# Optimization experiments

Measured on AMD Instinct MI355X. Metric: run time of the kernel, lower is better.

## Reference

```python
import jax, jax.numpy as jnp
import numpy as np

L, H = 3, 8
B, N, D, E = 4, 256, 128, 128
NH, EH1, EH2 = 512, 512, 512


def _ln(x, g, b):
    m = x.mean(-1, keepdims=True)
    v = ((x - m) ** 2).mean(-1, keepdims=True)
    return (x - m) * jax.lax.rsqrt(v + 1e-5) * g + b


def setup_inputs() -> dict:
    key = jax.random.key(0)
    ks = jax.random.split(key, 16)
    w = lambda k, *s: jax.random.normal(k, s, jnp.float32) * 0.02
    inp = {
        'node_features': jax.random.normal(ks[0], (B, N, D), jnp.float32),
        'edge_features': jax.random.normal(ks[1], (B, N, N, E), jnp.float32),
        'Wqkv_n': w(ks[2], L, D, 3 * D), 'bqkv_n': jnp.zeros((L, 3 * D)),
        'Wqkv_e': w(ks[3], L, E, 3 * D), 'bqkv_e': jnp.zeros((L, 3 * D)),
        'Wo': w(ks[4], L, D, D), 'bo': jnp.zeros((L, D)),
        'Wn1': w(ks[5], L, D, NH), 'bn1': jnp.zeros((L, NH)),
        'Wn2': w(ks[6], L, NH, D), 'bn2': jnp.zeros((L, D)),
        'ln1n_g': jnp.ones((L, D)), 'ln1n_b': jnp.zeros((L, D)),
        'ln2n_g': jnp.ones((L, D)), 'ln2n_b': jnp.zeros((L, D)),
        'We1a': w(ks[7], L, 2 * D + 2 * E, EH1), 'be1a': jnp.zeros((L, EH1)),
        'We1b': w(ks[8], L, EH1, E), 'be1b': jnp.zeros((L, E)),
        'We2a': w(ks[9], L, E, EH2), 'be2a': jnp.zeros((L, EH2)),
        'We2b': w(ks[10], L, EH2, E), 'be2b': jnp.zeros((L, E)),
        'ln1e_g': jnp.ones((L, E)), 'ln1e_b': jnp.zeros((L, E)),
        'ln2e_g': jnp.ones((L, E)), 'ln2e_b': jnp.zeros((L, E)),
    }
    return inp


def reference(node_features, edge_features, Wqkv_n, bqkv_n, Wqkv_e, bqkv_e, Wo, bo,
              Wn1, bn1, Wn2, bn2, ln1n_g, ln1n_b, ln2n_g, ln2n_b,
              We1a, be1a, We1b, be1b, We2a, be2a, We2b, be2b,
              ln1e_g, ln1e_b, ln2e_g, ln2e_b):
    n, e = node_features, edge_features
    b_, N_, D_ = n.shape
    hd = D_ // H
    scale = 1.0 / np.sqrt(hd).astype(np.float32)
    for l in range(Wqkv_n.shape[0]):
        # ---- edge-biased attention ----
        qkv_n = (n @ Wqkv_n[l] + bqkv_n[l]).reshape(b_, N_, H, 3 * hd).transpose(0, 2, 1, 3)  # B,H,N,3hd
        q_n, k_n, v_n = jnp.split(qkv_n, 3, axis=-1)
        qkv_e = (e @ Wqkv_e[l] + bqkv_e[l]).reshape(b_, N_, N_, H, 3 * hd).transpose(0, 3, 1, 2, 4)  # B,H,N,N,3hd
        q_e, k_e, v_e = jnp.split(qkv_e, 3, axis=-1)
        q = q_n[:, :, :, None, :] + q_e  # B,H,N,N,hd
        # NOTE: the original torch code overwrites k with q (`k = q.reshape(...)`),
        # so scores are the squared norm of q; k_n/k_e are dead code. Faithful.
        scores = jnp.einsum('bhijd,bhijd->bhij', q, q) * scale
        att = jax.nn.softmax(scores, axis=-1)
        v = v_n[:, :, None, :, :] + v_e  # B,H,N,N,hd
        out = jnp.einsum('bhij,bhijd->bhid', att, v)  # B,H,N,hd
        out = out.transpose(0, 2, 1, 3).reshape(b_, N_, D_) @ Wo[l] + bo[l]
        n = _ln(n + out, ln1n_g[l], ln1n_b[l])
        ff = jax.nn.relu(n @ Wn1[l] + bn1[l]) @ Wn2[l] + bn2[l]
        n = _ln(n + ff, ln2n_g[l], ln2n_b[l])
        # ---- edge update ----
        src = jnp.broadcast_to(n[:, None, :, :], (b_, N_, N_, D_))  # node j
        tgt = jnp.broadcast_to(n[:, :, None, :], (b_, N_, N_, D_))  # node i
        cat = jnp.concatenate([e, e.transpose(0, 2, 1, 3), src, tgt], axis=-1)
        e1 = jax.nn.relu(cat @ We1a[l] + be1a[l]) @ We1b[l] + be1b[l]
        e = _ln(e + e1, ln1e_g[l], ln1e_b[l])
        e2 = jax.nn.relu(e @ We2a[l] + be2a[l]) @ We2b[l] + be2b[l]
        e = _ln(e + e2, ln2e_g[l], ln2e_b[l])
    return n
```

## Files before the change

kernel.cpp:

```cpp
#include <hip/hip_runtime.h>

typedef unsigned short u16;
typedef __bf16 bf16x8 __attribute__((ext_vector_type(8)));
typedef float f32x4 __attribute__((ext_vector_type(4)));

#define NB 4
#define NN 256
#define DD 128
#define RNN 262144

__device__ __forceinline__ u16 f2b(float f) {
    unsigned u = __builtin_bit_cast(unsigned, f);
    unsigned rb = ((u >> 16) & 1u) + 0x7FFFu;
    return (u16)((u + rb) >> 16);
}
__device__ __forceinline__ float b2f(u16 u) {
    return __builtin_bit_cast(float, ((unsigned)u) << 16);
}

__device__ __forceinline__ void glds16(const void* g, void* l) {
    __builtin_amdgcn_global_load_lds((const __attribute__((address_space(1))) void*)g,
                                     (__attribute__((address_space(3))) void*)l, 16, 0, 0);
}

__global__ void prep_weights(const float* __restrict__ Wqkv_e, const float* __restrict__ bqkv_e,
                             const float* __restrict__ We1a, const float* __restrict__ We1b,
                             const float* __restrict__ We2a, const float* __restrict__ We2b,
                             u16* wqT, u16* wv, float* bqp, float* bvp,
                             u16* we1aT, u16* we1bT, u16* we2aT, u16* we2bT) {
    int l = blockIdx.z, sec = blockIdx.y;
    int idx = blockIdx.x * 256 + threadIdx.x;
    if (sec == 0) {
        if (idx < 16384) {
            int n = idx >> 7, k = idx & 127;
            int col = (n >> 4) * 48 + (n & 15);
            wqT[l * 16384 + n * 128 + k] = f2b(Wqkv_e[l * 49152 + k * 384 + col]);
        }
    } else if (sec == 1) {
        if (idx < 16384) {
            int k = idx >> 7, c = idx & 127;
            int col = (c >> 4) * 48 + 32 + (c & 15);
            wv[l * 16384 + k * 128 + c] = f2b(Wqkv_e[l * 49152 + k * 384 + col]);
        }
        if (idx < 128) {
            bqp[l * 128 + idx] = bqkv_e[l * 384 + (idx >> 4) * 48 + (idx & 15)];
            bvp[l * 128 + idx] = bqkv_e[l * 384 + (idx >> 4) * 48 + 32 + (idx & 15)];
        }
    } else if (sec == 2) {
        if (idx < 131072) {
            int n = idx >> 8, k = idx & 255;
            we1aT[l * 131072 + n * 256 + k] = f2b(We1a[l * 262144 + k * 512 + n]);
        }
    } else if (sec == 3) {
        if (idx < 65536) {
            int n = idx >> 9, k = idx & 511;
            we1bT[l * 65536 + n * 512 + k] = f2b(We1b[l * 65536 + k * 128 + n]);
        }
    } else if (sec == 4) {
        if (idx < 65536) {
            int n = idx >> 7, k = idx & 127;
            we2aT[l * 65536 + n * 128 + k] = f2b(We2a[l * 65536 + k * 512 + n]);
        }
    } else {
        if (idx < 65536) {
            int n = idx >> 9, k = idx & 511;
            we2bT[l * 65536 + n * 512 + k] = f2b(We2b[l * 65536 + k * 128 + n]);
        }
    }
}

__global__ void init_e(const float4* __restrict__ src, ushort4* __restrict__ dst) {
    const long n4 = 8388608;
    for (long i = (long)blockIdx.x * blockDim.x + threadIdx.x; i < n4; i += (long)gridDim.x * blockDim.x) {
        float4 v = src[i];
        ushort4 o;
        o.x = f2b(v.x); o.y = f2b(v.y); o.z = f2b(v.z); o.w = f2b(v.w);
        dst[i] = o;
    }
}

__global__ void init_n(const float* __restrict__ node, float* __restrict__ nf) {
    int i = blockIdx.x * 256 + threadIdx.x;
    if (i < 131072) nf[i] = node[i];
}

__launch_bounds__(512)
__global__ void pre_node_kernel(const float* __restrict__ nf, const float* __restrict__ We1a,
                                float* __restrict__ preS, float* __restrict__ preT) {
    __shared__ float nr[128];
    int tid = threadIdx.x;
    int row = blockIdx.x;
    if (tid < 128) nr[tid] = nf[(long)row * 128 + tid];
// ... 159 lines not shown
        g_s[(h0 + 6) * 128 + k] = a3;
    }
    __syncthreads();
    {
        int c = tid & 127, half = tid >> 7;
        int h = c >> 4;
        float a = 0.f;
        for (int j = half * 128; j < half * 128 + 128; ++j)
            a += s_s[h * 256 + j] * vn[((long)(b * NN + j)) * 128 + c];
        for (int k = half * 64; k < half * 64 + 64; ++k)
            a += g_s[h * 128 + k] * b2f(Wv[k * 128 + c]);
        part[tid] = a;
    }
    __syncthreads();
    if (tid < 128)
        attn_o[((long)(b * NN + i)) * 128 + tid] = part[tid] + part[128 + tid] + bvp[tid];
}

__launch_bounds__(256)
__global__ void node_kernel(const float* __restrict__ attn_o, float* __restrict__ nf,
                            const float* __restrict__ Wo, const float* __restrict__ bo,
                            const float* __restrict__ Wn1, const float* __restrict__ bn1,
                            const float* __restrict__ Wn2, const float* __restrict__ bn2,
                            const float* __restrict__ g1, const float* __restrict__ b1,
                            const float* __restrict__ g2, const float* __restrict__ b2) {
    __shared__ float ao[128], nr[128], n1[128], hb[512];
    __shared__ float red[8];
    int tid = threadIdx.x;
    int wid = tid >> 6, lane = tid & 63;
    long base = (long)blockIdx.x * 128;
    if (tid < 128) { ao[tid] = attn_o[base + tid]; nr[tid] = nf[base + tid]; }
    __syncthreads();
    float x = 0.f;
    if (tid < 128) {
        float a = bo[tid];
        #pragma unroll 8
        for (int k = 0; k < 128; ++k) a += ao[k] * Wo[k * 128 + tid];
        x = nr[tid] + a;
    }
    float s = (tid < 128) ? x : 0.f, q = (tid < 128) ? x * x : 0.f;
    #pragma unroll
    for (int mk = 1; mk <= 32; mk <<= 1) { s += __shfl_xor(s, mk); q += __shfl_xor(q, mk); }
    if (lane == 0) { red[wid * 2] = s; red[wid * 2 + 1] = q; }
    __syncthreads();
    float sum = red[0] + red[2] + red[4] + red[6];
    float sq  = red[1] + red[3] + red[5] + red[7];
    float mean = sum * (1.f / 128.f);
    float var = sq * (1.f / 128.f) - mean * mean;
    float rs = rsqrtf(var + 1e-5f);
    __syncthreads();
    if (tid < 128) n1[tid] = (x - mean) * rs * g1[tid] + b1[tid];
    __syncthreads();
    for (int c = tid; c < 512; c += 256) {
        float a = bn1[c];
        #pragma unroll 8
        for (int k = 0; k < 128; ++k) a += n1[k] * Wn1[k * 512 + c];
        hb[c] = a > 0.f ? a : 0.f;
    }
    __syncthreads();
    float y = 0.f;
    if (tid < 128) {
        float a = bn2[tid];
        #pragma unroll 8
        for (int k = 0; k < 512; ++k) a += hb[k] * Wn2[k * 128 + tid];
        y = n1[tid] + a;
    }
    float s2 = (tid < 128) ? y : 0.f, q2 = (tid < 128) ? y * y : 0.f;
    #pragma unroll
    for (int mk = 1; mk <= 32; mk <<= 1) { s2 += __shfl_xor(s2, mk); q2 += __shfl_xor(q2, mk); }
    if (lane == 0) { red[wid * 2] = s2; red[wid * 2 + 1] = q2; }
    __syncthreads();
    sum = red[0] + red[2] + red[4] + red[6];
    sq  = red[1] + red[3] + red[5] + red[7];
    mean = sum * (1.f / 128.f);
    var = sq * (1.f / 128.f) - mean * mean;
    rs = rsqrtf(var + 1e-5f);
    if (tid < 128) {
        float o = (y - mean) * rs * g2[tid] + b2[tid];
        nf[base + tid] = o;
    }
}

template<int KT1, int CAT>
__launch_bounds__(256, 2)
__global__ void fused_mlp2(const u16* __restrict__ W1T, const float* __restrict__ b1v,
                           const u16* __restrict__ W2T, const float* __restrict__ b2v,
                           const u16* __restrict__ ein, const u16* __restrict__ Aplain,
                           const u16* __restrict__ e_res,
                           const float* __restrict__ preS, const float* __restrict__ preT,
                           const float* __restrict__ lng, const float* __restrict__ lnb,
                           u16* __restrict__ e_dst) {
    __shared__ u16 A_lds[KT1 * 4096];
    __shared__ u16 Ws[8192];
    __shared__ u16 Hs[8192];

    const int K1 = KT1 * 64;
    int tid = threadIdx.x;
    int wid = tid >> 6, lane = tid & 63;
    long row0 = (long)blockIdx.x * 64;
    int b = (int)(row0 >> 16);
    int rem0 = (int)(row0 & 65535);
    int i_ = rem0 >> 8, j0 = rem0 & 255;
    int wn = wid >> 1, wrr = wid & 1;
    int wr2 = wid >> 1, wc2 = wid & 1;

    #pragma unroll
    for (int kt = 0; kt < KT1; ++kt) {
        #pragma unroll
        for (int p = 0; p < 2; ++p) {
            int r = p * 32 + (tid >> 3);
            int ch = tid & 7;
            const u16* src;
            if (CAT) {
                int seg = kt >> 1;
                int off = ((kt & 1) << 6) + ((ch ^ (r & 7)) << 3);
                long ridx = seg == 0 ? (long)(b * NN + i_) * NN + (j0 + r)
                                     : (long)(b * NN + (j0 + r)) * NN + i_;
                src = ein + ridx * DD + off;
            } else {
                src = Aplain + (row0 + r) * K1 + (kt << 6) + ((ch ^ (r & 7)) << 3);
            }
            glds16(src, (char*)A_lds + kt * 8192 + (p << 12) + (wid << 10));
        }
    }

    f32x4 z = {0.f, 0.f, 0.f, 0.f};
    f32x4 acc2[2][4];
    #pragma unroll
    for (int m = 0; m < 2; ++m)
        #pragma unroll
        for (int n = 0; n < 4; ++n) acc2[m][n] = z;

    for (int q = 0; q < 4; ++q) {
        int nq0 = q << 7;
        f32x4 acc1[4][2];
        #pragma unroll
        for (int mn = 0; mn < 4; ++mn) { acc1[mn][0] = z; acc1[mn][1] = z; }

        #pragma unroll
        for (int kt = 0; kt < KT1; ++kt) {
            #pragma unroll
            for (int pp = 0; pp < 4; ++pp) {
                int n = pp * 32 + (tid >> 3);
                int ch = tid & 7;
                const u16* src = W1T + (long)(nq0 + n) * K1 + (kt << 6) + ((ch ^ (n & 7)) << 3);
                glds16(src, (char*)Ws + (pp << 12) + (wid << 10));
            }
            __syncthreads();
            #pragma unroll
            for (int ks = 0; ks < 2; ++ks) {
                bf16x8 af[4], bfr[2];
                #pragma unroll
                for (int mn = 0; mn < 4; ++mn) {
                    int n = wn * 64 + mn * 16 + (lane & 15);
                    int ch = (ks * 4 + (lane >> 4)) ^ (n & 7);
                    af[mn] = *reinterpret_cast<const bf16x8*>(&Ws[n * 64 + ch * 8]);
                }
                #pragma unroll
                for (int mr = 0; mr < 2; ++mr) {
                    int r = wrr * 32 + mr * 16 + (lane & 15);
                    int ch = (ks * 4 + (lane >> 4)) ^ (r & 7);
                    bfr[mr] = *reinterpret_cast<const bf16x8*>(&A_lds[kt * 4096 + r * 64 + ch * 8]);
                }
                #pragma unroll
                for (int mn = 0; mn < 4; ++mn)
                    #pragma unroll
                    for (int mr = 0; mr < 2; ++mr)
                        acc1[mn][mr] = __builtin_amdgcn_mfma_f32_16x16x32_bf16(af[mn], bfr[mr], acc1[mn][mr], 0, 0, 0);
            }
            __syncthreads();
        }

        if (q == 3) {
            #pragma unroll
            for (int p = 0; p < 4; ++p) {
                int rr = p * 16 + (tid >> 4);
                const u16* src = e_res + (row0 + rr) * DD + ((tid & 15) << 3);
                glds16(src, (char*)A_lds + (p << 12) + (wid << 10));
            }
        }

        #pragma unroll
        for (int mn = 0; mn < 4; ++mn) {
            #pragma unroll
            for (int mr = 0; mr < 2; ++mr) {
                int nl0 = wn * 64 + mn * 16 + ((lane >> 4) << 2);
                int n0g = nq0 + nl0;
                int r = wrr * 32 + mr * 16 + (lane & 15);
                float4 bb = *reinterpret_cast<const float4*>(&b1v[n0g]);
                if (CAT) {
                    float4 pt = *reinterpret_cast<const float4*>(&preT[(long)(b * NN + i_) * 512 + n0g]);
                    float4 ps = *reinterpret_cast<const float4*>(&preS[(long)(b * NN + j0 + r) * 512 + n0g]);
                    bb.x += pt.x + ps.x; bb.y += pt.y + ps.y;
                    bb.z += pt.z + ps.z; bb.w += pt.w + ps.w;
                }
                float v0 = acc1[mn][mr][0] + bb.x; v0 = v0 > 0.f ? v0 : 0.f;
                float v1 = acc1[mn][mr][1] + bb.y; v1 = v1 > 0.f ? v1 : 0.f;
                float v2 = acc1[mn][mr][2] + bb.z; v2 = v2 > 0.f ? v2 : 0.f;
                float v3 = acc1[mn][mr][3] + bb.w; v3 = v3 > 0.f ? v3 : 0.f;
                uint2 pk;
                pk.x = (unsigned)f2b(v0) | ((unsigned)f2b(v1) << 16);
                pk.y = (unsigned)f2b(v2) | ((unsigned)f2b(v3) << 16);
                int c8 = nl0 >> 3;
                int cs = (c8 & 8) | ((c8 ^ r) & 7);
                *reinterpret_cast<uint2*>((char*)Hs + r * 256 + cs * 16 + (nl0 & 7) * 2) = pk;
            }
        }

        #pragma unroll
        for (int kt2 = 0; kt2 < 2; ++kt2) {
            #pragma unroll
            for (int pp = 0; pp < 4; ++pp) {
                int c = pp * 32 + (tid >> 3);
                int ch = tid & 7;
                const u16* src = W2T + (long)c * 512 + nq0 + (kt2 << 6) + ((ch ^ (c & 7)) << 3);
                glds16(src, (char*)Ws + (pp << 12) + (wid << 10));
            }
            __syncthreads();
            #pragma unroll
            for (int ks = 0; ks < 2; ++ks) {
                bf16x8 af2[2], bf2[4];
                #pragma unroll
                for (int m = 0; m < 2; ++m) {
                    int r = wr2 * 32 + m * 16 + (lane & 15);
                    int lk = kt2 * 64 + ks * 32 + ((lane >> 4) << 3);
                    int c8 = lk >> 3;
                    int cs = (c8 & 8) | ((c8 ^ r) & 7);
                    af2[m] = *reinterpret_cast<const bf16x8*>((char*)Hs + r * 256 + cs * 16);
                }
                #pragma unroll
                for (int n = 0; n < 4; ++n) {
                    int c = wc2 * 64 + n * 16 + (lane & 15);
                    int ch = (ks * 4 + (lane >> 4)) ^ (c & 7);
                    bf2[n] = *reinterpret_cast<const bf16x8*>(&Ws[c * 64 + ch * 8]);
                }
                #pragma unroll
                for (int m = 0; m < 2; ++m)
                    #pragma unroll
                    for (int n = 0; n < 4; ++n)
                        acc2[m][n] = __builtin_amdgcn_mfma_f32_16x16x32_bf16(af2[m], bf2[n], acc2[m][n], 0, 0, 0);
            }
            __syncthreads();
        }
    }

    float* psum = (float*)Hs;
    float* psq  = psum + 128;
    u16* eres_lds = A_lds;
    #pragma unroll
    for (int m = 0; m < 2; ++m) {
        float sv[4], qv[4];
        #pragma unroll
        for (int t = 0; t < 4; ++t) { sv[t] = 0.f; qv[t] = 0.f; }
        #pragma unroll
        for (int n = 0; n < 4; ++n) {
            int col = wc2 * 64 + n * 16 + (lane & 15);
            float bb = b2v[col];
            #pragma unroll
            for (int t = 0; t < 4; ++t) {
                int row = wr2 * 32 + m * 16 + ((lane >> 4) << 2) + t;
                float xv = acc2[m][n][t] + bb + b2f(eres_lds[row * 128 + col]);
                acc2[m][n][t] = xv;
                sv[t] += xv;
                qv[t] += xv * xv;
            }
        }
        #pragma unroll
        for (int mk = 1; mk <= 8; mk <<= 1)
            #pragma unroll
            for (int t = 0; t < 4; ++t) { sv[t] += __shfl_xor(sv[t], mk); qv[t] += __shfl_xor(qv[t], mk); }
        if ((lane & 15) == 0) {
            #pragma unroll
            for (int t = 0; t < 4; ++t) {
                int row = wr2 * 32 + m * 16 + ((lane >> 4) << 2) + t;
                psum[row * 2 + wc2] = sv[t];
                psq[row * 2 + wc2] = qv[t];
            }
        }
    }
    __syncthreads();
    #pragma unroll
    for (int m = 0; m < 2; ++m) {
        #pragma unroll
        for (int t = 0; t < 4; ++t) {
            int row = wr2 * 32 + m * 16 + ((lane >> 4) << 2) + t;
            float sum = psum[row * 2] + psum[row * 2 + 1];
            float sq  = psq[row * 2] + psq[row * 2 + 1];
            float mean = sum * (1.f / 128.f);
            float var = sq * (1.f / 128.f) - mean * mean;
            float rs = rsqrtf(var + 1e-5f);
            #pragma unroll
            for (int n = 0; n < 4; ++n) {
                int col = wc2 * 64 + n * 16 + (lane & 15);
                float o = (acc2[m][n][t] - mean) * rs * lng[col] + lnb[col];
                eres_lds[row * 128 + col] = f2b(o);
            }
        }
    }
    __syncthreads();
    #pragma unroll
    for (int p = 0; p < 4; ++p) {
        ulonglong2 v = *reinterpret_cast<const ulonglong2*>((char*)A_lds + (p << 12) + tid * 16);
        *reinterpret_cast<ulonglong2*>((char*)e_dst + row0 * 256 + (p << 12) + tid * 16) = v;
    }
}

extern "C" void kernel_launch(void* const* d_in, const int* in_sizes, int n_in,
                              void* d_out, int out_size, void* d_ws, size_t ws_size,
                              hipStream_t stream) {
    (void)in_sizes; (void)n_in; (void)out_size; (void)ws_size;
    const float* node   = (const float*)d_in[0];
    const float* edge   = (const float*)d_in[1];
    const float* Wqkv_n = (const float*)d_in[2];
    const float* bqkv_n = (const float*)d_in[3];
    const float* Wqkv_e = (const float*)d_in[4];
    const float* bqkv_e = (const float*)d_in[5];
    const float* Wo     = (const float*)d_in[6];
    const float* bo     = (const float*)d_in[7];
    const float* Wn1    = (const float*)d_in[8];
    const float* bn1    = (const float*)d_in[9];
    const float* Wn2    = (const float*)d_in[10];
    const float* bn2    = (const float*)d_in[11];
    const float* ln1n_g = (const float*)d_in[12];
    const float* ln1n_b = (const float*)d_in[13];
    const float* ln2n_g = (const float*)d_in[14];
    const float* ln2n_b = (const float*)d_in[15];
    const float* We1a   = (const float*)d_in[16];
    const float* be1a   = (const float*)d_in[17];
    const float* We1b   = (const float*)d_in[18];
    const float* be1b   = (const float*)d_in[19];
    const float* We2a   = (const float*)d_in[20];
    const float* be2a   = (const float*)d_in[21];
    const float* We2b   = (const float*)d_in[22];
    const float* be2b   = (const float*)d_in[23];
    const float* ln1e_g = (const float*)d_in[24];
    const float* ln1e_b = (const float*)d_in[25];
    const float* ln2e_g = (const float*)d_in[26];
    const float* ln2e_b = (const float*)d_in[27];

    size_t off = 0;
    char* wsb = (char*)d_ws;
    auto alloc = [&](size_t bytes) -> void* {
        void* p = wsb + off;
        off = (off + bytes + 255) & ~(size_t)255;
        return p;
    };
    u16* eb0      = (u16*)alloc((size_t)RNN * 128 * 2);
    u16* eb1      = (u16*)alloc((size_t)RNN * 128 * 2);
    float* scoresp= (float*)alloc((size_t)2097152 * 4);
    float* qn     = (float*)alloc(131072 * 4);
    float* vn     = (float*)alloc(131072 * 4);
    float* attn_o = (float*)alloc(131072 * 4);
    float* nf     = (float*)alloc(131072 * 4);
    float* preS   = (float*)alloc((size_t)1024 * 512 * 4);
    float* preT   = (float*)alloc((size_t)1024 * 512 * 4);
    u16* wqT      = (u16*)alloc(3 * 16384 * 2);
    u16* wv       = (u16*)alloc(3 * 16384 * 2);
    float* bqp    = (float*)alloc(3 * 128 * 4);
    float* bvp    = (float*)alloc(3 * 128 * 4);
    u16* we1aT    = (u16*)alloc(3 * 131072ull * 2);
    u16* we1bT    = (u16*)alloc(3 * 65536 * 2);
    u16* we2aT    = (u16*)alloc(3 * 65536 * 2);
    u16* we2bT    = (u16*)alloc(3 * 65536 * 2);

    {
        dim3 g(1024, 6, 3);
        prep_weights<<<g, 256, 0, stream>>>(Wqkv_e, bqkv_e, We1a, We1b, We2a, We2b,
                                            wqT, wv, bqp, bvp, we1aT, we1bT, we2aT, we2bT);
    }
    init_e<<<2048, 256, 0, stream>>>((const float4*)edge, (ushort4*)eb0);
    init_n<<<512, 256, 0, stream>>>(node, nf);

    for (int l = 0; l < 3; ++l) {
        u16* ein  = (l & 1) ? eb1 : eb0;
        u16* eout = (l & 1) ? eb0 : eb1;
        qkvn_kernel<<<1024, 256, 0, stream>>>(nf, Wqkv_n + l * 49152, bqkv_n + l * 384, qn, vn);
        scores_kernel<<<2048, 256, 0, stream>>>(ein, wqT + l * 16384, bqp + l * 128, qn, scoresp);
        attn_pv_kernel<<<1024, 256, 0, stream>>>(scoresp, ein, vn, wv + l * 16384, bvp + l * 128, attn_o);
        node_kernel<<<1024, 256, 0, stream>>>(attn_o, nf,
                                              Wo + l * 16384, bo + l * 128,
                                              Wn1 + l * 65536, bn1 + l * 512,
                                              Wn2 + l * 65536, bn2 + l * 128,
                                              ln1n_g + l * 128, ln1n_b + l * 128,
                                              ln2n_g + l * 128, ln2n_b + l * 128);
        pre_node_kernel<<<1024, 512, 0, stream>>>(nf, We1a + (size_t)l * 262144, preS, preT);
        fused_mlp2<4, 1><<<4096, 256, 0, stream>>>(we1aT + l * 131072, be1a + l * 512,
                                                   we1bT + l * 65536, be1b + l * 128,
                                                   ein, nullptr, ein, preS, preT,
                                                   ln1e_g + l * 128, ln1e_b + l * 128, eout);
        fused_mlp2<2, 0><<<4096, 256, 0, stream>>>(we2aT + l * 65536, be2a + l * 512,
                                                   we2bT + l * 65536, be2b + l * 128,
                                                   nullptr, eout, eout, nullptr, nullptr,
                                                   ln2e_g + l * 128, ln2e_b + l * 128, eout);
    }
    hipMemcpyAsync(d_out, nf, 131072 * sizeof(float), hipMemcpyDeviceToDevice, stream);
}
```

Measured before the change: 1.531 ms.

## Pipeline edge MLP weight tiles through triple-buffered LDS with interleaved GEMM phases

Rewrites the fused two-layer edge MLP kernel to stream weight tiles in 64-wide halves through a 3-stage LDS ring buffer. The next tile's global-to-LDS load is issued before computing on the current one, which hides load latency and cuts the barriers that used to bracket every tile. The residual is now read from the already-loaded input tile instead of being reloaded. Smaller LDS (half-size hidden buffer) allows 3 blocks/CU for the second MLP. The cost is more complex staging logic and more, finer-grained syncs.

```diff
diff --git a/kernel.cpp b/kernel.cpp
--- a/kernel.cpp
+++ b/kernel.cpp
@@ -8,6 +8,8 @@
 #define NN 256
 #define DD 128
 #define RNN 262144
+
+template<int N> struct IC { static constexpr int v = N; };
 
 __device__ __forceinline__ u16 f2b(float f) {
     unsigned u = __builtin_bit_cast(unsigned, f);
@@ -333,189 +335,217 @@
 }
 
 template<int KT1, int CAT>
-__launch_bounds__(256, 2)
-__global__ void fused_mlp2(const u16* __restrict__ W1T, const float* __restrict__ b1v,
+__launch_bounds__(256, (KT1 == 4) ? 2 : 3)
+__global__ void fused_mlp3(const u16* __restrict__ W1T, const float* __restrict__ b1v,
                            const u16* __restrict__ W2T, const float* __restrict__ b2v,
                            const u16* __restrict__ ein, const u16* __restrict__ Aplain,
-                           const u16* __restrict__ e_res,
                            const float* __restrict__ preS, const float* __restrict__ preT,
                            const float* __restrict__ lng, const float* __restrict__ lnb,
                            u16* __restrict__ e_dst) {
-    __shared__ u16 A_lds[KT1 * 4096];
-    __shared__ u16 Ws[8192];
-    __shared__ u16 Hs[8192];
-
-    const int K1 = KT1 * 64;
+    __shared__ __align__(16) u16 A_lds[KT1 * 4096];
+    __shared__ __align__(16) u16 ws[3 * 4096];
+    __shared__ __align__(16) u16 Hs[4096];
+
+    constexpr int K1 = KT1 * 64;
     int tid = threadIdx.x;
     int wid = tid >> 6, lane = tid & 63;
     long row0 = (long)blockIdx.x * 64;
     int b = (int)(row0 >> 16);
     int rem0 = (int)(row0 & 65535);
     int i_ = rem0 >> 8, j0 = rem0 & 255;
-    int wn = wid >> 1, wrr = wid & 1;
-    int wr2 = wid >> 1, wc2 = wid & 1;
-
-    #pragma unroll
-    for (int kt = 0; kt < KT1; ++kt) {
-        #pragma unroll
-        for (int p = 0; p < 2; ++p) {
-            int r = p * 32 + (tid >> 3);
+    int wa = wid >> 1, wb = wid & 1;
+
+    int stg = 0, rdS = 0;
+
+    auto SW1 = [&](int qq, int kt, int nh) {
+        char* dst = (char*)ws + stg * 8192; stg = (stg + 1) % 3;
+        #pragma unroll
+        for (int pp = 0; pp < 2; ++pp) {
+            int nl = pp * 32 + (tid >> 3);
+            int ch = tid & 7;
+            const u16* src = W1T + (long)((qq << 7) + nh * 64 + nl) * K1 + (kt << 6) + ((ch ^ (nl & 7)) << 3);
+            glds16(src, dst + (pp << 12) + (wid << 10));
+        }
+    };
+    auto SW2 = [&](int qq, int nh, int ch2) {
+        char* dst = (char*)ws + stg * 8192; stg = (stg + 1) % 3;
+        #pragma unroll
+        for (int pp = 0; pp < 2; ++pp) {
+            int cl = pp * 32 + (tid >> 3);
+            int ch = tid & 7;
+            const u16* src = W2T + (long)(ch2 * 64 + cl) * 512 + (qq << 7) + nh * 64 + ((ch ^ (cl & 7)) << 3);
+            glds16(src, dst + (pp << 12) + (wid << 10));
+        }
+    };
+
+    f32x4 z = {0.f, 0.f, 0.f, 0.f};
+    f32x4 acc1[2][2][2], acc2[2][2][2];
+    #pragma unroll
+    for (int a = 0; a < 2; ++a)
+        #pragma unroll
+        for (int m = 0; m < 2; ++m)
+            #pragma unroll
+            for (int n = 0; n < 2; ++n) { acc1[a][m][n] = z; acc2[a][m][n] = z; }
+
+    #pragma unroll
+    for (int kt = 0; kt < KT1; ++kt)
+        #pragma unroll
+        for (int pp = 0; pp < 2; ++pp) {
+            int r = pp * 32 + (tid >> 3);
             int ch = tid & 7;
             const u16* src;
-            if (CAT) {
-                int seg = kt >> 1;
-                int off = ((kt & 1) << 6) + ((ch ^ (r & 7)) << 3);
-                long ridx = seg == 0 ? (long)(b * NN + i_) * NN + (j0 + r)
+            if constexpr (CAT) {
+                long ridx = (kt < 2) ? (long)(b * NN + i_) * NN + (j0 + r)
                                      : (long)(b * NN + (j0 + r)) * NN + i_;
-                src = ein + ridx * DD + off;
+                src = ein + ridx * DD + ((kt & 1) << 6) + ((ch ^ (r & 7)) << 3);
             } else {
                 src = Aplain + (row0 + r) * K1 + (kt << 6) + ((ch ^ (r & 7)) << 3);
             }
-            glds16(src, (char*)A_lds + kt * 8192 + (p << 12) + (wid << 10));
-        }
-    }
-
-    f32x4 z = {0.f, 0.f, 0.f, 0.f};
-    f32x4 acc2[2][4];
-    #pragma unroll
-    for (int m = 0; m < 2; ++m)
-        #pragma unroll
-        for (int n = 0; n < 4; ++n) acc2[m][n] = z;
-
-    for (int q = 0; q < 4; ++q) {
+            glds16(src, (char*)A_lds + kt * 8192 + (pp << 12) + (wid << 10));
+        }
+    SW1(0, 0, 0);
+    SW1(0, 0, 1);
+    __syncthreads();
+
+    auto G1c = [&](int kt, auto nhc) {
+        constexpr int nh = decltype(nhc)::v;
+        const u16* w = ws + rdS * 4096; rdS = (rdS + 1) % 3;
+        #pragma unroll
+        for (int ks = 0; ks < 2; ++ks) {
+            bf16x8 af[2], bfr[2];
+            #pragma unroll
+            for (int mn = 0; mn < 2; ++mn) {
+                int nl = wa * 32 + mn * 16 + (lane & 15);
+                int ch = (ks * 4 + (lane >> 4)) ^ (nl & 7);
+                af[mn] = *reinterpret_cast<const bf16x8*>(&w[nl * 64 + ch * 8]);
+            }
+            #pragma unroll
+            for (int mr = 0; mr < 2; ++mr) {
+                int r = wb * 32 + mr * 16 + (lane & 15);
+                int ch = (ks * 4 + (lane >> 4)) ^ (r & 7);
+                bfr[mr] = *reinterpret_cast<const bf16x8*>(&A_lds[kt * 4096 + r * 64 + ch * 8]);
+            }
+            #pragma unroll
+            for (int mn = 0; mn < 2; ++mn)
+                #pragma unroll
+                for (int mr = 0; mr < 2; ++mr)
+                    acc1[nh][mn][mr] = __builtin_amdgcn_mfma_f32_16x16x32_bf16(af[mn], bfr[mr], acc1[nh][mn][mr], 0, 0, 0);
+        }
+    };
+
+    auto EPIc = [&](auto nhc, int q) {
+        constexpr int nh = decltype(nhc)::v;
         int nq0 = q << 7;
-        f32x4 acc1[4][2];
-        #pragma unroll
-        for (int mn = 0; mn < 4; ++mn) { acc1[mn][0] = z; acc1[mn][1] = z; }
-
-        #pragma unroll
-        for (int kt = 0; kt < KT1; ++kt) {
-            #pragma unroll
-            for (int pp = 0; pp < 4; ++pp) {
-                int n = pp * 32 + (tid >> 3);
-                int ch = tid & 7;
-                const u16* src = W1T + (long)(nq0 + n) * K1 + (kt << 6) + ((ch ^ (n & 7)) << 3);
-                glds16(src, (char*)Ws + (pp << 12) + (wid << 10));
-            }
-            __syncthreads();
-            #pragma unroll
-            for (int ks = 0; ks < 2; ++ks) {
-                bf16x8 af[4], bfr[2];
-                #pragma unroll
-                for (int mn = 0; mn < 4; ++mn) {
-                    int n = wn * 64 + mn * 16 + (lane & 15);
-                    int ch = (ks * 4 + (lane >> 4)) ^ (n & 7);
-                    af[mn] = *reinterpret_cast<const bf16x8*>(&Ws[n * 64 + ch * 8]);
+        #pragma unroll
+        for (int mn = 0; mn < 2; ++mn) {
+            int nl0 = wa * 32 + mn * 16 + ((lane >> 4) << 2);
+            int n0g = nq0 + nh * 64 + nl0;
+            float4 bb = *reinterpret_cast<const float4*>(&b1v[n0g]);
+            if constexpr (CAT) {
+                float4 pt = *reinterpret_cast<const float4*>(&preT[(long)(b * NN + i_) * 512 + n0g]);
+                bb.x += pt.x; bb.y += pt.y; bb.z += pt.z; bb.w += pt.w;
+            }
+            #pragma unroll
+            for (int mr = 0; mr < 2; ++mr) {
+                int r = wb * 32 + mr * 16 + (lane & 15);
+                float b0 = bb.x, b1_ = bb.y, b2_ = bb.z, b3 = bb.w;
+                if constexpr (CAT) {
+                    float4 ps = *reinterpret_cast<const float4*>(&preS[(long)(b * NN + j0 + r) * 512 + n0g]);
+                    b0 += ps.x; b1_ += ps.y; b2_ += ps.z; b3 += ps.w;
                 }
-                #pragma unroll
-                for (int mr = 0; mr < 2; ++mr) {
-                    int r = wrr * 32 + mr * 16 + (lane & 15);
-                    int ch = (ks * 4 + (lane >> 4)) ^ (r & 7);
-                    bfr[mr] = *reinterpret_cast<const bf16x8*>(&A_lds[kt * 4096 + r * 64 + ch * 8]);
-                }
-                #pragma unroll
-                for (int mn = 0; mn < 4; ++mn)
-                    #pragma unroll
-                    for (int mr = 0; mr < 2; ++mr)
-                        acc1[mn][mr] = __builtin_amdgcn_mfma_f32_16x16x32_bf16(af[mn], bfr[mr], acc1[mn][mr], 0, 0, 0);
-            }
-            __syncthreads();
-        }
-
-        if (q == 3) {
-            #pragma unroll
-            for (int p = 0; p < 4; ++p) {
-                int rr = p * 16 + (tid >> 4);
-                const u16* src = e_res + (row0 + rr) * DD + ((tid & 15) << 3);
-                glds16(src, (char*)A_lds + (p << 12) + (wid << 10));
-            }
-        }
-
-        #pragma unroll
-        for (int mn = 0; mn < 4; ++mn) {
-            #pragma unroll
-            for (int mr = 0; mr < 2; ++mr) {
-                int nl0 = wn * 64 + mn * 16 + ((lane >> 4) << 2);
-                int n0g = nq0 + nl0;
-                int r = wrr * 32 + mr * 16 + (lane & 15);
-                float4 bb = *reinterpret_cast<const float4*>(&b1v[n0g]);
-                if (CAT) {
-                    float4 pt = *reinterpret_cast<const float4*>(&preT[(long)(b * NN + i_) * 512 + n0g]);
-                    float4 ps = *reinterpret_cast<const float4*>(&preS[(long)(b * NN + j0 + r) * 512 + n0g]);
-                    bb.x += pt.x + ps.x; bb.y += pt.y + ps.y;
-                    bb.z += pt.z + ps.z; bb.w += pt.w + ps.w;
-                }
-                float v0 = acc1[mn][mr][0] + bb.x; v0 = v0 > 0.f ? v0 : 0.f;
-                float v1 = acc1[mn][mr][1] + bb.y; v1 = v1 > 0.f ? v1 : 0.f;
-                float v2 = acc1[mn][mr][2] + bb.z; v2 = v2 > 0.f ? v2 : 0.f;
-                float v3 = acc1[mn][mr][3] + bb.w; v3 = v3 > 0.f ? v3 : 0.f;
+                float v0 = acc1[nh][mn][mr][0] + b0; v0 = v0 > 0.f ? v0 : 0.f;
+                float v1 = acc1[nh][mn][mr][1] + b1_; v1 = v1 > 0.f ? v1 : 0.f;
+                float v2 = acc1[nh][mn][mr][2] + b2_; v2 = v2 > 0.f ? v2 : 0.f;
+                float v3 = acc1[nh][mn][mr][3] + b3; v3 = v3 > 0.f ? v3 : 0.f;
                 uint2 pk;
                 pk.x = (unsigned)f2b(v0) | ((unsigned)f2b(v1) << 16);
                 pk.y = (unsigned)f2b(v2) | ((unsigned)f2b(v3) << 16);
                 int c8 = nl0 >> 3;
-                int cs = (c8 & 8) | ((c8 ^ r) & 7);
-                *reinterpret_cast<uint2*>((char*)Hs + r * 256 + cs * 16 + (nl0 & 7) * 2) = pk;
-            }
-        }
-
-        #pragma unroll
-        for (int kt2 = 0; kt2 < 2; ++kt2) {
-            #pragma unroll
-            for (int pp = 0; pp < 4; ++pp) {
-                int c = pp * 32 + (tid >> 3);
-                int ch = tid & 7;
-                const u16* src = W2T + (long)c * 512 + nq0 + (kt2 << 6) + ((ch ^ (c & 7)) << 3);
-                glds16(src, (char*)Ws + (pp << 12) + (wid << 10));
-            }
-            __syncthreads();
-            #pragma unroll
-            for (int ks = 0; ks < 2; ++ks) {
-                bf16x8 af2[2], bf2[4];
+                int cs = (c8 ^ (r & 7)) & 7;
+                *reinterpret_cast<uint2*>((char*)Hs + r * 128 + cs * 16 + (nl0 & 7) * 2) = pk;
+                acc1[nh][mn][mr] = z;
+            }
+        }
+    };
+
+    auto G2c = [&](auto chc) {
+        constexpr int ch2 = decltype(chc)::v;
+        const u16* w = ws + rdS * 4096; rdS = (rdS + 1) % 3;
+        #pragma unroll
+        for (int ks = 0; ks < 2; ++ks) {
+            bf16x8 af2[2], bf2[2];
+            #pragma unroll
+            for (int mr = 0; mr < 2; ++mr) {
+                int r = wb * 32 + mr * 16 + (lane & 15);
+                int c8 = ks * 4 + (lane >> 4);
+                int cs = (c8 ^ (r & 7)) & 7;
+                af2[mr] = *reinterpret_cast<const bf16x8*>((const char*)Hs + r * 128 + cs * 16);
+            }
+            #pragma unroll
+            for (int mn = 0; mn < 2; ++mn) {
+                int cl = wa * 32 + mn * 16 + (lane & 15);
+                int chn = (ks * 4 + (lane >> 4)) ^ (cl & 7);
+                bf2[mn] = *reinterpret_cast<const bf16x8*>(&w[cl * 64 + chn * 8]);
+            }
+            #pragma unroll
+            for (int mr = 0; mr < 2; ++mr)
                 #pragma unroll
-                for (int m = 0; m < 2; ++m) {
-                    int r = wr2 * 32 + m * 16 + (lane & 15);
-                    int lk = kt2 * 64 + ks * 32 + ((lane >> 4) << 3);
-                    int c8 = lk >> 3;
-                    int cs = (c8 & 8) | ((c8 ^ r) & 7);
-                    af2[m] = *reinterpret_cast<const bf16x8*>((char*)Hs + r * 256 + cs * 16);
-                }
-                #pragma unroll
-                for (int n = 0; n < 4; ++n) {
-                    int c = wc2 * 64 + n * 16 + (lane & 15);
-                    int ch = (ks * 4 + (lane >> 4)) ^ (c & 7);
-                    bf2[n] = *reinterpret_cast<const bf16x8*>(&Ws[c * 64 + ch * 8]);
-                }
-                #pragma unroll
-                for (int m = 0; m < 2; ++m)
-                    #pragma unroll
-                    for (int n = 0; n < 4; ++n)
-                        acc2[m][n] = __builtin_amdgcn_mfma_f32_16x16x32_bf16(af2[m], bf2[n], acc2[m][n], 0, 0, 0);
-            }
-            __syncthreads();
-        }
+                for (int mn = 0; mn < 2; ++mn)
+                    acc2[ch2][mn][mr] = __builtin_amdgcn_mfma_f32_16x16x32_bf16(af2[mr], bf2[mn], acc2[ch2][mn][mr], 0, 0, 0);
+        }
+    };
+
+    for (int q = 0; q < 4; ++q) {
+        #pragma unroll
+        for (int kt = 0; kt < KT1; ++kt) {
+            {
+                int s = 2 * kt;
+                if (s < 2 * KT1 - 2) SW1(q, (s + 2) >> 1, (s + 2) & 1);
+                else                 SW2(q, 0, 0);
+                G1c(kt, IC<0>{});
+                __syncthreads();
+            }
+            {
+                int s = 2 * kt + 1;
+                if (s < 2 * KT1 - 2) SW1(q, (s + 2) >> 1, (s + 2) & 1);
+                else                 SW2(q, 0, 1);
+                G1c(kt, IC<1>{});
+                __syncthreads();
+            }
+        }
+        SW2(q, 1, 0); EPIc(IC<0>{}, q); __syncthreads();
+        G2c(IC<0>{});                   __syncthreads();
+        SW2(q, 1, 1); G2c(IC<1>{});     __syncthreads();
+        if (q < 3) SW1(q + 1, 0, 0);
+        EPIc(IC<1>{}, q);               __syncthreads();
+        G2c(IC<0>{});                   __syncthreads();
+        if (q < 3) SW1(q + 1, 0, 1);
+        G2c(IC<1>{});                   __syncthreads();
     }
 
     float* psum = (float*)Hs;
     float* psq  = psum + 128;
-    u16* eres_lds = A_lds;
-    #pragma unroll
-    for (int m = 0; m < 2; ++m) {
-        float sv[4], qv[4];
-        #pragma unroll
-        for (int t = 0; t < 4; ++t) { sv[t] = 0.f; qv[t] = 0.f; }
-        #pragma unroll
-        for (int n = 0; n < 4; ++n) {
-            int col = wc2 * 64 + n * 16 + (lane & 15);
-            float bb = b2v[col];
-            #pragma unroll
-            for (int t = 0; t < 4; ++t) {
-                int row = wr2 * 32 + m * 16 + ((lane >> 4) << 2) + t;
-                float xv = acc2[m][n][t] + bb + b2f(eres_lds[row * 128 + col]);
-                acc2[m][n][t] = xv;
-                sv[t] += xv;
-                qv[t] += xv * xv;
-            }
-        }
+    #pragma unroll
+    for (int mr = 0; mr < 2; ++mr) {
+        float sv[4] = {0.f, 0.f, 0.f, 0.f}, qv[4] = {0.f, 0.f, 0.f, 0.f};
+        #pragma unroll
+        for (int ch2 = 0; ch2 < 2; ++ch2)
+            #pragma unroll
+            for (int mn = 0; mn < 2; ++mn) {
+                int col = ch2 * 64 + wa * 32 + mn * 16 + (lane & 15);
+                float bb = b2v[col];
+                int kk = col & 63;
+                int kreg = col >> 6;
+                #pragma unroll
+                for (int t = 0; t < 4; ++t) {
+                    int row = wb * 32 + mr * 16 + ((lane >> 4) << 2) + t;
+                    float er = b2f(A_lds[kreg * 4096 + row * 64 + (((kk >> 3) ^ (row & 7)) << 3) + (kk & 7)]);
+                    float x = acc2[ch2][mn][mr][t] + bb + er;
+                    acc2[ch2][mn][mr][t] = x;
+                    sv[t] += x;
+                    qv[t] += x * x;
+                }
+            }
         #pragma unroll
         for (int mk = 1; mk <= 8; mk <<= 1)
             #pragma unroll
@@ -523,36 +553,41 @@
         if ((lane & 15) == 0) {
             #pragma unroll
             for (int t = 0; t < 4; ++t) {
-                int row = wr2 * 32 + m * 16 + ((lane >> 4) << 2) + t;
-                psum[row * 2 + wc2] = sv[t];
-                psq[row * 2 + wc2] = qv[t];
-            }
-        }
-    }
-    __syncthreads();
-    #pragma unroll
-    for (int m = 0; m < 2; ++m) {
+                int row = wb * 32 + mr * 16 + ((lane >> 4) << 2) + t;
+                psum[row * 2 + wa] = sv[t];
+                psq[row * 2 + wa] = qv[t];
+            }
+        }
+    }
+    __syncthreads();
+    u16* rp;
+    if constexpr (KT1 == 4) rp = A_lds + 8192;
+    else                    rp = ws;
+    #pragma unroll
+    for (int mr = 0; mr < 2; ++mr) {
         #pragma unroll
         for (int t = 0; t < 4; ++t) {
-            int row = wr2 * 32 + m * 16 + ((lane >> 4) << 2) + t;
+            int row = wb * 32 + mr * 16 + ((lane >> 4) << 2) + t;
             float sum = psum[row * 2] + psum[row * 2 + 1];
             float sq  = psq[row * 2] + psq[row * 2 + 1];
             float mean = sum * (1.f / 128.f);
             float var = sq * (1.f / 128.f) - mean * mean;
             float rs = rsqrtf(var + 1e-5f);
             #pragma unroll
-            for (int n = 0; n < 4; ++n) {
-                int col = wc2 * 64 + n * 16 + (lane & 15);
-                float o = (acc2[m][n][t] - mean) * rs * lng[col] + lnb[col];
-                eres_lds[row * 128 + col] = f2b(o);
-            }
-        }
-    }
-    __syncthreads();
-    #pragma unroll
-    for (int p = 0; p < 4; ++p) {
-        ulonglong2 v = *reinterpret_cast<const ulonglong2*>((char*)A_lds + (p << 12) + tid * 16);
-        *reinterpret_cast<ulonglong2*>((char*)e_dst + row0 * 256 + (p << 12) + tid * 16) = v;
+            for (int ch2 = 0; ch2 < 2; ++ch2)
+                #pragma unroll
+                for (int mn = 0; mn < 2; ++mn) {
+                    int col = ch2 * 64 + wa * 32 + mn * 16 + (lane & 15);
+                    float o = (acc2[ch2][mn][mr][t] - mean) * rs * lng[col] + lnb[col];
+                    rp[row * 128 + col] = f2b(o);
+                }
+        }
+    }
+    __syncthreads();
+    #pragma unroll
+    for (int pp = 0; pp < 4; ++pp) {
+        ulonglong2 v = *reinterpret_cast<const ulonglong2*>((char*)rp + (pp << 12) + tid * 16);
+        *reinterpret_cast<ulonglong2*>((char*)e_dst + row0 * 256 + (pp << 12) + tid * 16) = v;
     }
 }
 
@@ -635,13 +670,13 @@
                                               ln1n_g + l * 128, ln1n_b + l * 128,
                                               ln2n_g + l * 128, ln2n_b + l * 128);
         pre_node_kernel<<<1024, 512, 0, stream>>>(nf, We1a + (size_t)l * 262144, preS, preT);
-        fused_mlp2<4, 1><<<4096, 256, 0, stream>>>(we1aT + l * 131072, be1a + l * 512,
+        fused_mlp3<4, 1><<<4096, 256, 0, stream>>>(we1aT + l * 131072, be1a + l * 512,
                                                    we1bT + l * 65536, be1b + l * 128,
-                                                   ein, nullptr, ein, preS, preT,
+                                                   ein, nullptr, preS, preT,
                                                    ln1e_g + l * 128, ln1e_b + l * 128, eout);
-        fused_mlp2<2, 0><<<4096, 256, 0, stream>>>(we2aT + l * 65536, be2a + l * 512,
+        fused_mlp3<2, 0><<<4096, 256, 0, stream>>>(we2aT + l * 65536, be2a + l * 512,
                                                    we2bT + l * 65536, be2b + l * 128,
-                                                   nullptr, eout, eout, nullptr, nullptr,
+                                                   nullptr, eout, nullptr, nullptr,
                                                    ln2e_g + l * 128, ln2e_b + l * 128, eout);
     }
     hipMemcpyAsync(d_out, nf, 131072 * sizeof(float), hipMemcpyDeviceToDevice, stream);
```

Result: slower. 1.680 ms (+9.7%).

## Double-buffer weight tiles in fused edge MLP and reuse staged input as residual

Applied to the files above, without the earlier changes.

The fused two-layer edge MLP kernel now keeps two LDS weight buffers and prefetches the next W1/W2 tile while the current one feeds MFMA, using raw barriers and vmcnt waits in place of full __syncthreads. The separate global reload of the residual edge tile is removed; the residual is read from the already-staged, swizzled A tile in LDS. The preT bias load is hoisted out of the inner row loop. This adds LDS use (an extra 16KB buffer), which may lower occupancy, and relies on hand-placed waitcnt values being correct.

```diff
diff --git a/kernel.cpp b/kernel.cpp
--- a/kernel.cpp
+++ b/kernel.cpp
@@ -334,18 +334,17 @@
 
 template<int KT1, int CAT>
 __launch_bounds__(256, 2)
-__global__ void fused_mlp2(const u16* __restrict__ W1T, const float* __restrict__ b1v,
+__global__ void fused_mlp4(const u16* __restrict__ W1T, const float* __restrict__ b1v,
                            const u16* __restrict__ W2T, const float* __restrict__ b2v,
                            const u16* __restrict__ ein, const u16* __restrict__ Aplain,
-                           const u16* __restrict__ e_res,
                            const float* __restrict__ preS, const float* __restrict__ preT,
                            const float* __restrict__ lng, const float* __restrict__ lnb,
                            u16* __restrict__ e_dst) {
-    __shared__ u16 A_lds[KT1 * 4096];
-    __shared__ u16 Ws[8192];
-    __shared__ u16 Hs[8192];
-
-    const int K1 = KT1 * 64;
+    __shared__ __align__(16) u16 A_lds[KT1 * 4096];
+    __shared__ __align__(16) u16 Wsl[2][8192];
+    __shared__ __align__(16) u16 Hs[8192];
+
+    constexpr int K1 = KT1 * 64;
     int tid = threadIdx.x;
     int wid = tid >> 6, lane = tid & 63;
     long row0 = (long)blockIdx.x * 64;
@@ -355,49 +354,68 @@
     int wn = wid >> 1, wrr = wid & 1;
     int wr2 = wid >> 1, wc2 = wid & 1;
 
-    #pragma unroll
-    for (int kt = 0; kt < KT1; ++kt) {
-        #pragma unroll
-        for (int p = 0; p < 2; ++p) {
-            int r = p * 32 + (tid >> 3);
+    auto stageW1 = [&](int qq, int kt, int slot) {
+        char* dst = (char*)Wsl[slot];
+        #pragma unroll
+        for (int pp = 0; pp < 4; ++pp) {
+            int nl = pp * 32 + (tid >> 3);
+            int ch = tid & 7;
+            const u16* src = W1T + (long)((qq << 7) + nl) * K1 + (kt << 6) + ((ch ^ (nl & 7)) << 3);
+            glds16(src, dst + (pp << 12) + (wid << 10));
+        }
+    };
+    auto stageW2 = [&](int qq, int kt2, int slot) {
+        char* dst = (char*)Wsl[slot];
+        #pragma unroll
+        for (int pp = 0; pp < 4; ++pp) {
+            int cl = pp * 32 + (tid >> 3);
+            int ch = tid & 7;
+            const u16* src = W2T + (long)cl * 512 + (qq << 7) + (kt2 << 6) + ((ch ^ (cl & 7)) << 3);
+            glds16(src, dst + (pp << 12) + (wid << 10));
+        }
+    };
+
+    f32x4 z = {0.f, 0.f, 0.f, 0.f};
+    f32x4 acc2[2][4];
+    #pragma unroll
+    for (int m = 0; m < 2; ++m)
+        #pragma unroll
+        for (int n = 0; n < 4; ++n) acc2[m][n] = z;
+
+    #pragma unroll
+    for (int kt = 0; kt < KT1; ++kt)
+        #pragma unroll
+        for (int pp = 0; pp < 2; ++pp) {
+            int r = pp * 32 + (tid >> 3);
             int ch = tid & 7;
             const u16* src;
-            if (CAT) {
-                int seg = kt >> 1;
-                int off = ((kt & 1) << 6) + ((ch ^ (r & 7)) << 3);
-                long ridx = seg == 0 ? (long)(b * NN + i_) * NN + (j0 + r)
+            if constexpr (CAT) {
+                long ridx = (kt < 2) ? (long)(b * NN + i_) * NN + (j0 + r)
                                      : (long)(b * NN + (j0 + r)) * NN + i_;
-                src = ein + ridx * DD + off;
+                src = ein + ridx * DD + ((kt & 1) << 6) + ((ch ^ (r & 7)) << 3);
             } else {
                 src = Aplain + (row0 + r) * K1 + (kt << 6) + ((ch ^ (r & 7)) << 3);
             }
-            glds16(src, (char*)A_lds + kt * 8192 + (p << 12) + (wid << 10));
-        }
-    }
-
-    f32x4 z = {0.f, 0.f, 0.f, 0.f};
-    f32x4 acc2[2][4];
-    #pragma unroll
-    for (int m = 0; m < 2; ++m)
-        #pragma unroll
-        for (int n = 0; n < 4; ++n) acc2[m][n] = z;
+            glds16(src, (char*)A_lds + kt * 8192 + (pp << 12) + (wid << 10));
+        }
+    stageW1(0, 0, 0);
 
     for (int q = 0; q < 4; ++q) {
-        int nq0 = q << 7;
         f32x4 acc1[4][2];
         #pragma unroll
         for (int mn = 0; mn < 4; ++mn) { acc1[mn][0] = z; acc1[mn][1] = z; }
 
         #pragma unroll
         for (int kt = 0; kt < KT1; ++kt) {
-            #pragma unroll
-            for (int pp = 0; pp < 4; ++pp) {
-                int n = pp * 32 + (tid >> 3);
-                int ch = tid & 7;
-                const u16* src = W1T + (long)(nq0 + n) * K1 + (kt << 6) + ((ch ^ (n & 7)) << 3);
-                glds16(src, (char*)Ws + (pp << 12) + (wid << 10));
-            }
-            __syncthreads();
+            __builtin_amdgcn_s_barrier();
+            __builtin_amdgcn_sched_barrier(0);
+            if (kt + 1 < KT1) stageW1(q, kt + 1, (kt + 1) & 1);
+            else              stageW2(q, 0, (kt + 1) & 1);
+            __builtin_amdgcn_sched_barrier(0);
+            asm volatile("s_waitcnt vmcnt(4)" ::: "memory");
+            __builtin_amdgcn_sched_barrier(0);
+            const u16* w = Wsl[kt & 1];
+            __builtin_amdgcn_s_setprio(1);
             #pragma unroll
             for (int ks = 0; ks < 2; ++ks) {
                 bf16x8 af[4], bfr[2];
@@ -405,7 +423,7 @@
                 for (int mn = 0; mn < 4; ++mn) {
                     int n = wn * 64 + mn * 16 + (lane & 15);
                     int ch = (ks * 4 + (lane >> 4)) ^ (n & 7);
-                    af[mn] = *reinterpret_cast<const bf16x8*>(&Ws[n * 64 + ch * 8]);
+                    af[mn] = *reinterpret_cast<const bf16x8*>(&w[n * 64 + ch * 8]);
                 }
                 #pragma unroll
                 for (int mr = 0; mr < 2; ++mr) {
@@ -419,36 +437,30 @@
                     for (int mr = 0; mr < 2; ++mr)
                         acc1[mn][mr] = __builtin_amdgcn_mfma_f32_16x16x32_bf16(af[mn], bfr[mr], acc1[mn][mr], 0, 0, 0);
             }
-            __syncthreads();
-        }
-
-        if (q == 3) {
-            #pragma unroll
-            for (int p = 0; p < 4; ++p) {
-                int rr = p * 16 + (tid >> 4);
-                const u16* src = e_res + (row0 + rr) * DD + ((tid & 15) << 3);
-                glds16(src, (char*)A_lds + (p << 12) + (wid << 10));
-            }
+            __builtin_amdgcn_s_setprio(0);
         }
 
         #pragma unroll
         for (int mn = 0; mn < 4; ++mn) {
+            int nl0 = wn * 64 + mn * 16 + ((lane >> 4) << 2);
+            int n0g = (q << 7) + nl0;
+            float4 bb = *reinterpret_cast<const float4*>(&b1v[n0g]);
+            if constexpr (CAT) {
+                float4 pt = *reinterpret_cast<const float4*>(&preT[(long)(b * NN + i_) * 512 + n0g]);
+                bb.x += pt.x; bb.y += pt.y; bb.z += pt.z; bb.w += pt.w;
+            }
             #pragma unroll
             for (int mr = 0; mr < 2; ++mr) {
-                int nl0 = wn * 64 + mn * 16 + ((lane >> 4) << 2);
-                int n0g = nq0 + nl0;
                 int r = wrr * 32 + mr * 16 + (lane & 15);
-                float4 bb = *reinterpret_cast<const float4*>(&b1v[n0g]);
-                if (CAT) {
-                    float4 pt = *reinterpret_cast<const float4*>(&preT[(long)(b * NN + i_) * 512 + n0g]);
+                float b0 = bb.x, b1_ = bb.y, b2_ = bb.z, b3 = bb.w;
+                if constexpr (CAT) {
                     float4 ps = *reinterpret_cast<const float4*>(&preS[(long)(b * NN + j0 + r) * 512 + n0g]);
-                    bb.x += pt.x + ps.x; bb.y += pt.y + ps.y;
-                    bb.z += pt.z + ps.z; bb.w += pt.w + ps.w;
+                    b0 += ps.x; b1_ += ps.y; b2_ += ps.z; b3 += ps.w;
                 }
-                float v0 = acc1[mn][mr][0] + bb.x; v0 = v0 > 0.f ? v0 : 0.f;
-                float v1 = acc1[mn][mr][1] + bb.y; v1 = v1 > 0.f ? v1 : 0.f;
-                float v2 = acc1[mn][mr][2] + bb.z; v2 = v2 > 0.f ? v2 : 0.f;
-                float v3 = acc1[mn][mr][3] + bb.w; v3 = v3 > 0.f ? v3 : 0.f;
+                float v0 = acc1[mn][mr][0] + b0; v0 = v0 > 0.f ? v0 : 0.f;
+                float v1 = acc1[mn][mr][1] + b1_; v1 = v1 > 0.f ? v1 : 0.f;
+                float v2 = acc1[mn][mr][2] + b2_; v2 = v2 > 0.f ? v2 : 0.f;
+                float v3 = acc1[mn][mr][3] + b3; v3 = v3 > 0.f ? v3 : 0.f;
                 uint2 pk;
                 pk.x = (unsigned)f2b(v0) | ((unsigned)f2b(v1) << 16);
                 pk.y = (unsigned)f2b(v2) | ((unsigned)f2b(v3) << 16);
@@ -457,17 +469,20 @@
                 *reinterpret_cast<uint2*>((char*)Hs + r * 256 + cs * 16 + (nl0 & 7) * 2) = pk;
             }
         }
+        asm volatile("s_waitcnt lgkmcnt(0)" ::: "memory");
 
         #pragma unroll
         for (int kt2 = 0; kt2 < 2; ++kt2) {
-            #pragma unroll
-            for (int pp = 0; pp < 4; ++pp) {
-                int c = pp * 32 + (tid >> 3);
-                int ch = tid & 7;
-                const u16* src = W2T + (long)c * 512 + nq0 + (kt2 << 6) + ((ch ^ (c & 7)) << 3);
-                glds16(src, (char*)Ws + (pp << 12) + (wid << 10));
-            }
-            __syncthreads();
+            __builtin_amdgcn_s_barrier();
+            __builtin_amdgcn_sched_barrier(0);
+            if (kt2 == 0)      stageW2(q, 1, 1);
+            else if (q < 3)    stageW1(q + 1, 0, 0);
+            __builtin_amdgcn_sched_barrier(0);
+            if (kt2 == 0 || q < 3) asm volatile("s_waitcnt vmcnt(4)" ::: "memory");
+            else                   asm volatile("s_waitcnt vmcnt(0)" ::: "memory");
+            __builtin_amdgcn_sched_barrier(0);
+            const u16* w = Wsl[kt2 & 1];
+            __builtin_amdgcn_s_setprio(1);
             #pragma unroll
             for (int ks = 0; ks < 2; ++ks) {
                 bf16x8 af2[2], bf2[4];
@@ -477,13 +492,13 @@
                     int lk = kt2 * 64 + ks * 32 + ((lane >> 4) << 3);
                     int c8 = lk >> 3;
                     int cs = (c8 & 8) | ((c8 ^ r) & 7);
-                    af2[m] = *reinterpret_cast<const bf16x8*>((char*)Hs + r * 256 + cs * 16);
+                    af2[m] = *reinterpret_cast<const bf16x8*>((const char*)Hs + r * 256 + cs * 16);
                 }
                 #pragma unroll
                 for (int n = 0; n < 4; ++n) {
                     int c = wc2 * 64 + n * 16 + (lane & 15);
-                    int ch = (ks * 4 + (lane >> 4)) ^ (c & 7);
-                    bf2[n] = *reinterpret_cast<const bf16x8*>(&Ws[c * 64 + ch * 8]);
+                    int chn = (ks * 4 + (lane >> 4)) ^ (c & 7);
+                    bf2[n] = *reinterpret_cast<const bf16x8*>(&w[c * 64 + chn * 8]);
                 }
                 #pragma unroll
                 for (int m = 0; m < 2; ++m)
@@ -491,29 +506,29 @@
                     for (int n = 0; n < 4; ++n)
                         acc2[m][n] = __builtin_amdgcn_mfma_f32_16x16x32_bf16(af2[m], bf2[n], acc2[m][n], 0, 0, 0);
             }
-            __syncthreads();
-        }
-    }
+            __builtin_amdgcn_s_setprio(0);
+        }
+    }
+    __syncthreads();
 
     float* psum = (float*)Hs;
     float* psq  = psum + 128;
-    u16* eres_lds = A_lds;
     #pragma unroll
     for (int m = 0; m < 2; ++m) {
-        float sv[4], qv[4];
-        #pragma unroll
-        for (int t = 0; t < 4; ++t) { sv[t] = 0.f; qv[t] = 0.f; }
+        float sv[4] = {0.f, 0.f, 0.f, 0.f}, qv[4] = {0.f, 0.f, 0.f, 0.f};
         #pragma unroll
         for (int n = 0; n < 4; ++n) {
             int col = wc2 * 64 + n * 16 + (lane & 15);
             float bb = b2v[col];
+            int kk = col & 63, kreg = col >> 6;
             #pragma unroll
             for (int t = 0; t < 4; ++t) {
                 int row = wr2 * 32 + m * 16 + ((lane >> 4) << 2) + t;
-                float xv = acc2[m][n][t] + bb + b2f(eres_lds[row * 128 + col]);
-                acc2[m][n][t] = xv;
-                sv[t] += xv;
-                qv[t] += xv * xv;
+                float er = b2f(A_lds[kreg * 4096 + row * 64 + (((kk >> 3) ^ (row & 7)) << 3) + (kk & 7)]);
+                float x = acc2[m][n][t] + bb + er;
+                acc2[m][n][t] = x;
+                sv[t] += x;
+                qv[t] += x * x;
             }
         }
         #pragma unroll
@@ -530,6 +545,9 @@
         }
     }
     __syncthreads();
+    u16* rp;
+    if constexpr (KT1 == 4) rp = A_lds + 8192;
+    else                    rp = Wsl[0];
     #pragma unroll
     for (int m = 0; m < 2; ++m) {
         #pragma unroll
@@ -544,15 +562,15 @@
             for (int n = 0; n < 4; ++n) {
                 int col = wc2 * 64 + n * 16 + (lane & 15);
                 float o = (acc2[m][n][t] - mean) * rs * lng[col] + lnb[col];
-                eres_lds[row * 128 + col] = f2b(o);
-            }
-        }
-    }
-    __syncthreads();
-    #pragma unroll
-    for (int p = 0; p < 4; ++p) {
-        ulonglong2 v = *reinterpret_cast<const ulonglong2*>((char*)A_lds + (p << 12) + tid * 16);
-        *reinterpret_cast<ulonglong2*>((char*)e_dst + row0 * 256 + (p << 12) + tid * 16) = v;
+                rp[row * 128 + col] = f2b(o);
+            }
+        }
+    }
+    __syncthreads();
+    #pragma unroll
+    for (int pp = 0; pp < 4; ++pp) {
+        ulonglong2 v = *reinterpret_cast<const ulonglong2*>((char*)rp + (pp << 12) + tid * 16);
+        *reinterpret_cast<ulonglong2*>((char*)e_dst + row0 * 256 + (pp << 12) + tid * 16) = v;
     }
 }
 
@@ -635,13 +653,13 @@
                                               ln1n_g + l * 128, ln1n_b + l * 128,
                                               ln2n_g + l * 128, ln2n_b + l * 128);
         pre_node_kernel<<<1024, 512, 0, stream>>>(nf, We1a + (size_t)l * 262144, preS, preT);
-        fused_mlp2<4, 1><<<4096, 256, 0, stream>>>(we1aT + l * 131072, be1a + l * 512,
+        fused_mlp4<4, 1><<<4096, 256, 0, stream>>>(we1aT + l * 131072, be1a + l * 512,
                                                    we1bT + l * 65536, be1b + l * 128,
-                                                   ein, nullptr, ein, preS, preT,
+                                                   ein, nullptr, preS, preT,
                                                    ln1e_g + l * 128, ln1e_b + l * 128, eout);
-        fused_mlp2<2, 0><<<4096, 256, 0, stream>>>(we2aT + l * 65536, be2a + l * 512,
+        fused_mlp4<2, 0><<<4096, 256, 0, stream>>>(we2aT + l * 65536, be2a + l * 512,
                                                    we2bT + l * 65536, be2b + l * 128,
-                                                   nullptr, eout, eout, nullptr, nullptr,
+                                                   nullptr, eout, nullptr, nullptr,
                                                    ln2e_g + l * 128, ln2e_b + l * 128, eout);
     }
     hipMemcpyAsync(d_out, nf, 131072 * sizeof(float), hipMemcpyDeviceToDevice, stream);
```

Measured after the change: 1.521 ms. No clear change (-0.7%).
